# Performance work log

Hardware: AMD Instinct MI355X
Metric: run time of the kernel (lower is better)

## Reference

```python
import jax, jax.numpy as jnp
import numpy as np

PS = 3
B, C, H, W = 4, 256, 64, 64
IMG = 256
_MEAN = np.array([0.485, 0.456, 0.406], dtype=np.float32).reshape(1, 3, 1, 1)
_STD = np.array([0.229, 0.224, 0.225], dtype=np.float32).reshape(1, 3, 1, 1)


def setup_inputs() -> dict:
    key = jax.random.key(0)
    ks = jax.random.split(key, 16)
    d = {
        "dense_features1": jax.random.normal(ks[0], (B, C, H, W), jnp.float32),
        "dense_features2": jax.random.normal(ks[1], (B, C, H, W), jnp.float32),
        "img_ref_hr": jax.random.uniform(ks[2], (B, 3, IMG, IMG), jnp.float32),
        "w1_1": jax.random.normal(ks[3], (64, 3, 3, 3), jnp.float32) * 0.05,
        "b1_1": jnp.zeros((64,), jnp.float32),
        "w1_2": jax.random.normal(ks[4], (64, 64, 3, 3), jnp.float32) * 0.05,
        "b1_2": jnp.zeros((64,), jnp.float32),
        "w2_1": jax.random.normal(ks[5], (128, 64, 3, 3), jnp.float32) * 0.05,
        "b2_1": jnp.zeros((128,), jnp.float32),
        "w2_2": jax.random.normal(ks[6], (128, 128, 3, 3), jnp.float32) * 0.05,
        "b2_2": jnp.zeros((128,), jnp.float32),
        "w3_1": jax.random.normal(ks[7], (256, 128, 3, 3), jnp.float32) * 0.05,
        "b3_1": jnp.zeros((256,), jnp.float32),
    }
    return d


def _conv(x, w, b):
    y = jax.lax.conv_general_dilated(x, w, (1, 1), "SAME",
                                     dimension_numbers=("NCHW", "OIHW", "NCHW"))
    return y + b[None, :, None, None]


def _pool(x):
    return jax.lax.reduce_window(x, -jnp.inf, jax.lax.max, (1, 1, 2, 2), (1, 1, 2, 2), "VALID")


def _vgg(img, w11, b11, w12, b12, w21, b21, w22, b22, w31, b31):
    x = (img - _MEAN) / _STD  # ImageNet input norm (use_input_norm=True)
    r11 = jax.nn.relu(_conv(x, w11, b11))
    x = _pool(jax.nn.relu(_conv(r11, w12, b12)))
    r21 = jax.nn.relu(_conv(x, w21, b21))
    x = _pool(jax.nn.relu(_conv(r21, w22, b22)))
    r31 = jax.nn.relu(_conv(x, w31, b31))
    return r11, r21, r31


def _l2n(f):  # per-pixel channel L2 normalize (F.normalize dim=0, eps=1e-12)
    return f / jnp.maximum(jnp.linalg.norm(f, axis=0, keepdims=True), 1e-12)


def _patches(f):  # (c,h,w) -> (nh*nw, c*PS*PS), row-major patch order
    c, h, w = f.shape
    nh, nw = h - PS + 1, w - PS + 1
    cols = jnp.stack([f[:, i:i + nh, j:j + nw] for i in range(PS) for j in range(PS)], axis=1)
    return cols.reshape(c * PS * PS, nh * nw).T


def _match(fin, fref):
    fin, fref = _l2n(fin), _l2n(fref)
    nh, nw = fin.shape[1] - PS + 1, fin.shape[2] - PS + 1
    p_in = _patches(fin)
    p_ref = _patches(fref)
    p_ref = p_ref / (jnp.linalg.norm(p_ref, axis=1, keepdims=True) + 1e-5)  # is_norm
    corr = p_in @ p_ref.T  # (N_in, N_ref) patch correlation
    return jnp.argmax(corr, axis=1).reshape(nh, nw)


def _index_to_flow(idx):  # (nh,nw) int -> (nh+2, nw+2, 2) float flow
    nh, nw = idx.shape
    fw = (idx % nw).astype(jnp.float32) - jnp.arange(nw, dtype=jnp.float32)[None, :]
    fh = (idx // nw).astype(jnp.float32) - jnp.arange(nh, dtype=jnp.float32)[:, None]
    flow = jnp.stack([fw, fh], axis=-1)
    return jnp.pad(flow, ((0, 2), (0, 2), (0, 0)))


def _shift9(flow, s):  # 9 down/right shifts with zero fill -> (9,H,W,2)
    Hh, Ww, _ = flow.shape
    outs = [jnp.pad(flow, ((i * s, 0), (j * s, 0), (0, 0)))[:Hh, :Ww]
            for i in range(3) for j in range(3)]
    return jnp.stack(outs, axis=0)


def _per_sample(fin, fref):
    flow3 = _index_to_flow(_match(fin, fref))
    off3 = _shift9(flow3, 1)
    flow2 = jnp.repeat(jnp.repeat(flow3, 2, axis=0), 2, axis=1) * 2.0
    off2 = _shift9(flow2, 2)
    flow1 = jnp.repeat(jnp.repeat(flow3, 4, axis=0), 4, axis=1) * 4.0
    off1 = _shift9(flow1, 4)
    return off1, off2, off3


def reference(dense_features1, dense_features2, img_ref_hr,
              w1_1, b1_1, w1_2, b1_2, w2_1, b2_1, w2_2, b2_2, w3_1, b3_1):
    off1, off2, off3 = jax.vmap(_per_sample)(dense_features1, dense_features2)
    r11, r21, r31 = _vgg(img_ref_hr, w1_1, b1_1, w1_2, b1_2, w2_1, b2_1, w2_2, b2_2, w3_1, b3_1)
    # pre_offset['relu1_1'/'relu2_1'/'relu3_1'], img_ref_feat['relu1_1'/'relu2_1'/'relu3_1']
    return (off1, off2, off3, r11, r21, r31)
```

## Files before the change

### kernel.cpp

```cpp
#include <hip/hip_runtime.h>

typedef __attribute__((ext_vector_type(4))) float f32x4;
typedef __attribute__((ext_vector_type(8))) short s16x8;

#define OFF1_OFF 0
#define OFF2_OFF 4718592
#define OFF3_OFF 5898240
#define R11_OFF  6193152
#define R21_OFF  22970368
#define R31_OFF  31358976

__device__ __forceinline__ ushort f2bf(float x) {
  union { float f; uint u; } c; c.f = x;
  uint r = c.u + 0x7FFFu + ((c.u >> 16) & 1u);
  return (ushort)(r >> 16);
}
__device__ __forceinline__ float bfval(ushort h) {
  union { uint u; float f; } c; c.u = ((uint)h) << 16;
  return c.f;
}

__global__ __launch_bounds__(256)
void k_normalize(const float* __restrict__ f1, const float* __restrict__ f2,
                 ushort* __restrict__ n1b, ushort* __restrict__ n2b) {
  __shared__ uint ldsu[64 * 256];
  float* red = (float*)ldsu;
  float* inv = (float*)ldsu + 256;
  const int t = threadIdx.x, x = t & 63, cg = t >> 6;
  const int h = blockIdx.x, b = blockIdx.y;
  const float* in = blockIdx.z ? f2 : f1;
  ushort* op = blockIdx.z ? n2b : n1b;
  const size_t base = (size_t)b * 256 * 4096 + (size_t)h * 64 + x;
  float vals[64];
  float s = 0.f;
  #pragma unroll
  for (int ci = 0; ci < 64; ++ci) {
    float v = in[base + (size_t)(cg * 64 + ci) * 4096];
    vals[ci] = v;
    s = fmaf(v, v, s);
  }
  red[t] = s;
  __syncthreads();
  if (t < 64) {
    float tot = red[t] + red[64 + t] + red[128 + t] + red[192 + t];
    inv[t] = 1.0f / fmaxf(sqrtf(tot), 1e-12f);
  }
  __syncthreads();
  const float iv = inv[x];
  __syncthreads();
  #pragma unroll
  for (int j = 0; j < 32; ++j) {
    float v0 = vals[2 * j] * iv, v1 = vals[2 * j + 1] * iv;
    ushort h0 = f2bf(v0), h1 = f2bf(v1);
    ushort l0 = f2bf(v0 - bfval(h0)), l1 = f2bf(v1 - bfval(h1));
    int cc = (cg << 1) + (j >> 4);
    int i = j & 15;
    int qh = cc * 32 + i, ql = cc * 32 + 16 + i;
    ldsu[x * 256 + (qh ^ (x & 31))] = (uint)h0 | ((uint)h1 << 16);
    ldsu[x * 256 + (ql ^ (x & 31))] = (uint)l0 | ((uint)l1 << 16);
  }
  __syncthreads();
  uint* og = (uint*)(op + ((size_t)b * 4096 + h * 64) * 512);
  #pragma unroll
  for (int it = 0; it < 64; ++it) {
    int idx = it * 256 + t;
    int p = idx >> 8, q = idx & 255;
    og[idx] = ldsu[p * 256 + (q ^ (p & 31))];
  }
}

__global__ __launch_bounds__(256)
void k_pgemm_mfma(const ushort* __restrict__ Ab0, const ushort* __restrict__ Bb0,
                  float* __restrict__ P0) {
  __shared__ __align__(16) ushort As[128 * 64];
  __shared__ __align__(16) ushort Bs[128 * 64];
  const int t = threadIdx.x;
  const int bz = blockIdx.z;
  const ushort* Ab = Ab0 + (size_t)bz * 2097152;
  const ushort* Bb = Bb0 + (size_t)bz * 2097152;
  float* P = P0 + (size_t)bz * 16777216;
  const int u0 = blockIdx.y * 128, v0 = blockIdx.x * 128;
  const int lane = t & 63, wv = t >> 6;
  const int wm = wv >> 1, wn = wv & 1;
  const int lr = lane & 15, lk = lane >> 4;
  int rowv[4], slotv[4];
  #pragma unroll
  for (int i = 0; i < 4; ++i) { int e = t + i * 256; rowv[i] = e >> 3; slotv[i] = e & 7; }
  s16x8 ra[4], rb[4];
  #pragma unroll
  for (int i = 0; i < 4; ++i) {
    ra[i] = *(const s16x8*)(Ab + ((size_t)(u0 + rowv[i])) * 512 + slotv[i] * 8);
    rb[i] = *(const s16x8*)(Bb + ((size_t)(v0 + rowv[i])) * 512 + slotv[i] * 8);
  }
  f32x4 acc[4][4];
  #pragma unroll
  for (int mt = 0; mt < 4; ++mt)
    #pragma unroll
    for (int nt = 0; nt < 4; ++nt) {
      f32x4 z = {0.f, 0.f, 0.f, 0.f};
      acc[mt][nt] = z;
    }

  #pragma unroll 1
  for (int cc = 0; cc < 8; ++cc) {
    __syncthreads();
    #pragma unroll
    for (int i = 0; i < 4; ++i) {
      *(s16x8*)(As + ((rowv[i] << 3) + (slotv[i] ^ (rowv[i] & 7))) * 8) = ra[i];
      *(s16x8*)(Bs + ((rowv[i] << 3) + (slotv[i] ^ (rowv[i] & 7))) * 8) = rb[i];
    }
    __syncthreads();
    if (cc < 7) {
      #pragma unroll
      for (int i = 0; i < 4; ++i) {
        ra[i] = *(const s16x8*)(Ab + ((size_t)(u0 + rowv[i])) * 512 + (cc + 1) * 64 + slotv[i] * 8);
        rb[i] = *(const s16x8*)(Bb + ((size_t)(v0 + rowv[i])) * 512 + (cc + 1) * 64 + slotv[i] * 8);
      }
    }
    s16x8 ah[4], al[4], bh[4], bl[4];
    #pragma unroll
    for (int mt = 0; mt < 4; ++mt) {
      int row = wm * 64 + mt * 16 + lr;
      ah[mt] = *(const s16x8*)(As + ((row << 3) + (lk ^ (row & 7))) * 8);
      al[mt] = *(const s16x8*)(As + ((row << 3) + ((4 + lk) ^ (row & 7))) * 8);
    }
    #pragma unroll
    for (int nt = 0; nt < 4; ++nt) {
      int row = wn * 64 + nt * 16 + lr;
      bh[nt] = *(const s16x8*)(Bs + ((row << 3) + (lk ^ (row & 7))) * 8);
      bl[nt] = *(const s16x8*)(Bs + ((row << 3) + ((4 + lk) ^ (row & 7))) * 8);
    }
    #pragma unroll
    for (int mt = 0; mt < 4; ++mt)
      #pragma unroll
      for (int nt = 0; nt < 4; ++nt) {
        acc[mt][nt] = __builtin_amdgcn_mfma_f32_16x16x32_bf16(al[mt], bh[nt], acc[mt][nt], 0, 0, 0);
        acc[mt][nt] = __builtin_amdgcn_mfma_f32_16x16x32_bf16(ah[mt], bl[nt], acc[mt][nt], 0, 0, 0);
        acc[mt][nt] = __builtin_amdgcn_mfma_f32_16x16x32_bf16(ah[mt], bh[nt], acc[mt][nt], 0, 0, 0);
      }
  }
  const int plane = ((blockIdx.y * 2 + wm) << 6) + blockIdx.x * 2 + wn;
  float* Pp = P + (size_t)plane * 4096;
  #pragma unroll
  for (int mt = 0; mt < 4; ++mt)
    #pragma unroll
    for (int nt = 0; nt < 4; ++nt) {
      #pragma unroll
      for (int r = 0; r < 4; ++r)
        Pp[(mt * 16 + lk * 4 + r) * 64 + nt * 16 + lr] = acc[mt][nt][r];
    }
}

__global__ __launch_bounds__(256)
void k_corr(const float* __restrict__ P0, float* __restrict__ pv0,
            int* __restrict__ pi0) {
  __shared__ __align__(16) f32x4 Pl[3 * 1024];
  __shared__ float rv[256];
  __shared__ int   ri[256];
  const int t = threadIdx.x;
  const int orig = blockIdx.x;
  const int w = (orig & 7) * 1922 + (orig >> 3);
  const int bz = w / 3844;
  const int r2 = w % 3844;
  const int py = r2 / 62, qy = r2 % 62;
  const float* P = P0 + (size_t)bz * 16777216;
  float* pv = pv0 + (size_t)bz * 238328;
  int*   pi = pi0 + (size_t)bz * 238328;
  #pragma unroll
  for (int i = 0; i < 12; ++i) {
    int e = t + i * 256;
    int blk = e >> 10, rem = e & 1023;
    int px = rem >> 4, q4 = rem & 15;
    int pidx = (py + blk) * 64 + (qy + blk);
    f32x4 v = *(const f32x4*)(P + (size_t)pidx * 4096 + rem * 4);
    int slot = ((q4 + (px >> 4)) & 15) ^ (px & 15);
    Pl[blk * 1024 + px * 16 + slot] = v;
  }
  __syncthreads();
  const int px = t & 63, cg = t >> 6;
  #pragma unroll
  for (int j = 0; j < 4; ++j) {
    int c = cg * 4 + j;
    int slot = ((c + (px >> 4)) & 15) ^ (px & 15);
    int o = px * 16 + slot;
    Pl[o] = Pl[o] + Pl[1024 + o] + Pl[2048 + o];
  }
  __syncthreads();
  float bv = -3.4e38f; int bq = 0;
  if (px < 62) {
    const int q0 = cg * 16;
    const int nq = (cg < 3) ? 16 : 14;
    const int nch = (cg < 3) ? 5 : 4;
    float f[3][20];
    #pragma unroll
    for (int dj = 0; dj < 3; ++dj) {
      const int row = px + dj;
      const int rr = row >> 4, rm = row & 15;
      #pragma unroll
      for (int cc2 = 0; cc2 < 5; ++cc2) {
        if (cc2 < nch) {
          int c = cg * 4 + cc2;
          int slot = ((c + rr) & 15) ^ rm;
          f32x4 v = Pl[row * 16 + slot];
          f[dj][cc2 * 4 + 0] = v[0];
          f[dj][cc2 * 4 + 1] = v[1];
          f[dj][cc2 * 4 + 2] = v[2];
          f[dj][cc2 * 4 + 3] = v[3];
        }
      }
    }
    #pragma unroll
    for (int l = 0; l < 16; ++l) {
      if (l < nq) {
        float s = f[0][l] + f[1][l + 1] + f[2][l + 2];
        if (s > bv) { bv = s; bq = q0 + l; }
      }
    }
  }
  rv[t] = bv; ri[t] = bq;
  __syncthreads();
  if (t < 62) {
    float v = rv[t]; int q = ri[t];
    #pragma unroll
    for (int g = 1; g < 4; ++g) {
      float v2 = rv[g * 64 + t];
      if (v2 > v) { v = v2; q = ri[g * 64 + t]; }
    }
    const int n = py * 62 + t;
    pv[(size_t)n * 62 + qy] = v;
    pi[(size_t)n * 62 + qy] = qy * 62 + q;
  }
}

__global__ void k_argmax(const float* __restrict__ pv, const int* __restrict__ pi,
                         int* __restrict__ idxf) {
  int tid = blockIdx.x * 256 + threadIdx.x;
  if (tid >= 4 * 3844) return;
  const float* v = pv + (size_t)tid * 62;
  const int*  ii = pi + (size_t)tid * 62;
  float bv = v[0]; int bi = ii[0];
  for (int q = 1; q < 62; ++q) {
    float x = v[q];
    if (x > bv) { bv = x; bi = ii[q]; }
  }
  idxf[tid] = bi;
}

__global__ void k_flow_all(const int* __restrict__ idxf, float* __restrict__ out) {
  int gid = blockIdx.x * 256 + threadIdx.x;
  int Ho, lg, rel = gid;
  float* o;
  if (gid < 2359296)      { Ho = 256; lg = 2; o = out + OFF1_OFF; }
  else if (gid < 2949120) { Ho = 128; lg = 1; o = out + OFF2_OFF; rel -= 2359296; }
  else if (gid < 3096576) { Ho = 64;  lg = 0; o = out + OFF3_OFF; rel -= 2949120; }
  else return;
  const int x = rel % Ho;
  const int y = (rel / Ho) % Ho;
  const int s = (rel / (Ho * Ho)) % 9;
  const int b = rel / (Ho * Ho * 9);
  const int i = s / 3, j = s % 3;
  const int sc = 1 << lg;
  const int yy = y - i * sc, xx = x - j * sc;
  float fw = 0.f, fh = 0.f;
  if (yy >= 0 && xx >= 0) {
    const int r = yy >> lg, c = xx >> lg;
    if (r < 62 && c < 62) {
      const int id = idxf[b * 3844 + r * 62 + c];
      fw = (float)((id % 62 - c) * sc);
      fh = (float)((id / 62 - r) * sc);
    }
  }
  float2 ov = {fw, fh};
  *(float2*)(o + (size_t)rel * 2) = ov;
}

__global__ void k_wprep_all(const float* __restrict__ w12, const float* __restrict__ w21,
                            const float* __restrict__ w22, const float* __restrict__ w31,
                            ushort* __restrict__ o12, ushort* __restrict__ o21,
                            ushort* __restrict__ o22, ushort* __restrict__ o31) {
  int gid = blockIdx.x * 256 + threadIdx.x;
  const float* w; ushort* o; int CIN, rel;
  if (gid < 36864)        { w = w12; o = o12; CIN = 64;  rel = gid; }
  else if (gid < 110592)  { w = w21; o = o21; CIN = 64;  rel = gid - 36864; }
  else if (gid < 258048)  { w = w22; o = o22; CIN = 128; rel = gid - 110592; }
  else if (gid < 552960)  { w = w31; o = o31; CIN = 128; rel = gid - 258048; }
  else return;
  int ci = rel % CIN;
  int r = rel / CIN;
  int tap = r % 9;
  int oc = r / 9;
  o[((size_t)oc * 9 + tap) * CIN + ci] = f2bf(w[((size_t)oc * CIN + ci) * 9 + tap]);
}

__global__ void k_zb(ushort* __restrict__ a11, ushort* __restrict__ p1,
                     ushort* __restrict__ a21, ushort* __restrict__ p2) {
  int gid = blockIdx.x * 256 + threadIdx.x;
  if (gid >= 99072) return;
  int b = gid / 24768, r = gid % 24768;
  ushort* p; int Hp, Wp, C8, u;
  size_t stride;
  if (r < 8224)       { p = a11; Hp = 258; Wp = 258; C8 = 8;  stride = 4260096; u = r; }
  else if (r < 12352) { p = p1;  Hp = 130; Wp = 130; C8 = 8;  stride = 1081600; u = r - 8224; }
  else if (r < 20608) { p = a21; Hp = 130; Wp = 130; C8 = 16; stride = 2163200; u = r - 12352; }
  else                { p = p2;  Hp = 66;  Wp = 66;  C8 = 16; stride = 557568;  u = r - 20608; }
  int pos = u / C8, j = u % C8;
  int row, col;
  if (pos < Wp)            { row = 0;      col = pos; }
  else if (pos < 2 * Wp)   { row = Hp - 1; col = pos - Wp; }
  else { int q = pos - 2 * Wp; row = 1 + (q >> 1); col = (q & 1) ? (Wp - 1) : 0; }
  s16x8 z = {0, 0, 0, 0, 0, 0, 0, 0};
  *(s16x8*)(p + (size_t)b * stride + (((size_t)row * Wp + col) * C8 + j) * 8) = z;
}

__global__ __launch_bounds__(256)
void k_conv11(const float* __restrict__ img0, const float* __restrict__ w,
              const float* __restrict__ bias, float* __restrict__ outF0,
              ushort* __restrict__ outB0) {
  __shared__ float wl[1728];
  __shared__ float bl[64];
  const int t = threadIdx.x;
  const int b = blockIdx.y;
  const float* img = img0 + (size_t)b * 3 * 65536;
  float* outF = outF0 + (size_t)b * 64 * 65536;
  ushort* outB = outB0 + (size_t)b * 4260096;
  for (int i = t; i < 1728; i += 256) wl[i] = w[i];
  if (t < 64) bl[t] = bias[t];
  __syncthreads();
  const int x = t, y = blockIdx.x;
  const float mean[3] = {0.485f, 0.456f, 0.406f};
  const float stdv[3] = {0.229f, 0.224f, 0.225f};
  float v[27];
  #pragma unroll
  for (int c = 0; c < 3; ++c)
    #pragma unroll
    for (int dy = 0; dy < 3; ++dy)
      #pragma unroll
      for (int dx = 0; dx < 3; ++dx) {
        int iy = y + dy - 1, ix = x + dx - 1;
        float val = 0.f;
        if (iy >= 0 && iy < 256 && ix >= 0 && ix < 256)
          val = (img[((size_t)c * 256 + iy) * 256 + ix] - mean[c]) / stdv[c];
        v[c * 9 + dy * 3 + dx] = val;
      }
  float ov[64];
  #pragma unroll 4
  for (int oc = 0; oc < 64; ++oc) {
    float a = bl[oc];
    #pragma unroll
    for (int k = 0; k < 27; ++k) a = fmaf(wl[oc * 27 + k], v[k], a);
    a = fmaxf(a, 0.f);
    ov[oc] = a;
    outF[((size_t)oc * 256 + y) * 256 + x] = a;
  }
  uint* ob = (uint*)(outB + (((size_t)(y + 1) * 258 + (x + 1)) << 6));
  #pragma unroll
  for (int j = 0; j < 32; ++j)
    ob[j] = (uint)f2bf(ov[2 * j]) | ((uint)f2bf(ov[2 * j + 1]) << 16);
}

template <int CIN, bool POOL, bool WB16>
__global__ __launch_bounds__(256)
void k_mconv(const ushort* __restrict__ inb, const ushort* __restrict__ wB,
             const float* __restrict__ bias, float* __restrict__ outF,
             ushort* __restrict__ outB, int H, int W, int Cout,
             int inStride, int fStride, int bStride, int PW, int POut) {
  __shared__ __align__(16) char lds_raw[33792];
  ushort* As = (ushort*)lds_raw;
  float*  sm = (float*)lds_raw;
  const int t = threadIdx.x;
  const int bz = blockIdx.z;
  inb += (size_t)bz * inStride;
  outF += (size_t)bz * fStride;
  outB += (size_t)bz * bStride;
  const int xtiles = W >> 6;
  const int xt = blockIdx.x % xtiles;
  const int yp = blockIdx.x / xtiles;
  const int x0 = xt << 6, y0 = yp << 1;
  const int ocb = blockIdx.y << 6;
  const int lane = t & 63, wv = t >> 6;
  const int wm = wv >> 1, wn = wv & 1;
  const int lr = lane & 15, lk = lane >> 4;
  constexpr int NC2 = CIN / 64;

  f32x4 acc[4][2];
  #pragma unroll
  for (int mr = 0; mr < 4; ++mr)
    #pragma unroll
    for (int n = 0; n < 2; ++n) {
      f32x4 z = {0.f, 0.f, 0.f, 0.f};
      acc[mr][n] = z;
    }

  #pragma unroll 1
  for (int cc = 0; cc < NC2; ++cc) {
    __syncthreads();
    #pragma unroll
    for (int i = 0; i < 9; ++i) {
      int e = t + i * 256;
      if (e < 2112) {
        int pos = e >> 3;
        int gs = (e & 7) ^ (pos & 7);
        int hy = pos / 66, hx = pos - hy * 66;
        __builtin_amdgcn_global_load_lds(
            (const __attribute__((address_space(1))) void*)(
                inb + ((size_t)(y0 + hy) * PW + x0 + hx) * CIN + cc * 64 + gs * 8),
            (__attribute__((address_space(3))) void*)(As + (size_t)e * 8), 16, 0, 0);
      }
    }
    __syncthreads();
    #pragma unroll 3
    for (int tap = 0; tap < 9; ++tap) {
      const int dy = tap / 3, dx = tap % 3;
      s16x8 b0[2], b1[2];
      #pragma unroll
      for (int n = 0; n < 2; ++n) {
        const ushort* wp =
            wB + ((size_t)(ocb + wn * 32 + n * 16 + lr) * 9 + tap) * CIN + cc * 64 + lk * 8;
        b0[n] = *(const s16x8*)wp;
        b1[n] = *(const s16x8*)(wp + 32);
      }
      #pragma unroll
      for (int mr = 0; mr < 4; ++mr) {
        const int pos = (wm + dy) * 66 + mr * 16 + lr + dx;
        s16x8 a0 = *(const s16x8*)(As + ((pos << 3) + (lk ^ (pos & 7))) * 8);
        s16x8 a1 = *(const s16x8*)(As + ((pos << 3) + ((4 + lk) ^ (pos & 7))) * 8);
        #pragma unroll
        for (int n = 0; n < 2; ++n) {
          acc[mr][n] = __builtin_amdgcn_mfma_f32_16x16x32_bf16(a0, b0[n], acc[mr][n], 0, 0, 0);
          acc[mr][n] = __builtin_amdgcn_mfma_f32_16x16x32_bf16(a1, b1[n], acc[mr][n], 0, 0, 0);
        }
      }
    }
  }
  __syncthreads();
  #pragma unroll
  for (int mr = 0; mr < 4; ++mr)
    #pragma unroll
    for (int n = 0; n < 2; ++n) {
      const int oc = wn * 32 + n * 16 + lr;
      const float bs = bias[ocb + oc];
      #pragma unroll
      for (int r = 0; r < 4; ++r)
        sm[(wm * 64 + mr * 16 + lk * 4 + r) * 65 + oc] =
            fmaxf(acc[mr][n][r] + bs, 0.f);
    }
  __syncthreads();
  if (POOL) {
    #pragma unroll
    for (int i = 0; i < 4; ++i) {
      int e = t + i * 256;
      int op = e & 31, xo = e >> 5;
      int oc0 = op * 2;
      float m0 = fmaxf(fmaxf(sm[(xo * 2) * 65 + oc0], sm[(xo * 2 + 1) * 65 + oc0]),
                       fmaxf(sm[(64 + xo * 2) * 65 + oc0], sm[(64 + xo * 2 + 1) * 65 + oc0]));
      float m1 = fmaxf(fmaxf(sm[(xo * 2) * 65 + oc0 + 1], sm[(xo * 2 + 1) * 65 + oc0 + 1]),
                       fmaxf(sm[(64 + xo * 2) * 65 + oc0 + 1], sm[(64 + xo * 2 + 1) * 65 + oc0 + 1]));
      size_t pos = (size_t)(yp + 1) * POut + (x0 >> 1) + xo + 1;
      ((uint*)outB)[pos * (Cout >> 1) + ((ocb >> 1) + op)] =
          (uint)f2bf(m0) | ((uint)f2bf(m1) << 16);
    }
  } else {
    #pragma unroll
    for (int i = 0; i < 32; ++i) {
      int e = t + i * 256;
      int oc = e >> 7, sp = e & 127;
      outF[((size_t)(ocb + oc) * H + y0 + (sp >> 6)) * W + x0 + (sp & 63)] =
          sm[sp * 65 + oc];
    }
    if (WB16) {
      #pragma unroll
      for (int i = 0; i < 16; ++i) {
        int e = t + i * 256;
        int op = e & 31, sp = e >> 5;
        int oc0 = op * 2;
        float v0 = sm[sp * 65 + oc0], v1 = sm[sp * 65 + oc0 + 1];
        size_t pos = (size_t)(y0 + (sp >> 6) + 1) * POut + x0 + (sp & 63) + 1;
        ((uint*)outB)[pos * (Cout >> 1) + ((ocb >> 1) + op)] =
            (uint)f2bf(v0) | ((uint)f2bf(v1) << 16);
      }
    }
  }
}

extern "C" void kernel_launch(void* const* d_in, const int* in_sizes, int n_in,
                              void* d_out, int out_size, void* d_ws, size_t ws_size,
                              hipStream_t stream) {
  const float* df1 = (const float*)d_in[0];
  const float* df2 = (const float*)d_in[1];
  const float* img = (const float*)d_in[2];
  const float* w11 = (const float*)d_in[3];
  const float* b11 = (const float*)d_in[4];
  const float* w12 = (const float*)d_in[5];
  const float* b12 = (const float*)d_in[6];
  const float* w21 = (const float*)d_in[7];
  const float* b21 = (const float*)d_in[8];
  const float* w22 = (const float*)d_in[9];
  const float* b22 = (const float*)d_in[10];
  const float* w31 = (const float*)d_in[11];
  const float* b31 = (const float*)d_in[12];
  float* out = (float*)d_out;

  int* idxf = (int*)d_ws;
  ushort* w12b = (ushort*)(idxf + 15376);
  ushort* w21b = w12b + 36864;
  ushort* w22b = w21b + 73728;
  ushort* w31b = w22b + 147456;
  float* P4 = (float*)((char*)d_ws + (size_t)(4 << 20));
  ushort* a11s = (ushort*)P4;
  ushort* p1bs = a11s + 17040384;
  ushort* a21s = p1bs + 4326400;
  ushort* p2bs = a21s + 8652800;

  ushort* n1b = (ushort*)(out + R21_OFF);
  ushort* n2b = n1b + 8388608;
  float* pv = out + OFF1_OFF;
  int*   pi = (int*)(out + OFF1_OFF + 953312);

  k_normalize<<<dim3(64, 4, 2), 256, 0, stream>>>(df1, df2, n1b, n2b);
  k_wprep_all<<<2160, 256, 0, stream>>>(w12, w21, w22, w31, w12b, w21b, w22b, w31b);

  k_pgemm_mfma<<<dim3(32, 32, 4), 256, 0, stream>>>(n1b, n2b, P4);
  k_corr<<<15376, 256, 0, stream>>>(P4, pv, pi);
  k_argmax<<<61, 256, 0, stream>>>(pv, pi, idxf);

  k_zb<<<387, 256, 0, stream>>>(a11s, p1bs, a21s, p2bs);
  k_conv11<<<dim3(256, 4), 256, 0, stream>>>(img, w11, b11, out + R11_OFF, a11s);
  k_mconv<64, true, false><<<dim3(512, 1, 4), 256, 0, stream>>>(
      a11s, w12b, b12, nullptr, p1bs, 256, 256, 64, 4260096, 0, 1081600, 258, 130);
  k_mconv<64, false, true><<<dim3(128, 2, 4), 256, 0, stream>>>(
      p1bs, w21b, b21, out + R21_OFF, a21s, 128, 128, 128, 1081600, 2097152, 2163200, 130, 130);
  k_mconv<128, true, false><<<dim3(128, 2, 4), 256, 0, stream>>>(
      a21s, w22b, b22, nullptr, p2bs, 128, 128, 128, 2163200, 0, 557568, 130, 66);
  k_mconv<128, false, false><<<dim3(32, 4, 4), 256, 0, stream>>>(
      p2bs, w31b, b31, out + R31_OFF, nullptr, 64, 64, 256, 557568, 1048576, 0, 66, 0);

  k_flow_all<<<12096, 256, 0, stream>>>(idxf, out);
}
```

Baseline: 451.6 us.

## Double-buffer pgemm via direct global-to-LDS loads; coalesce conv11 bf16 stores through LDS

The correlation GEMM now stages A/B tiles with global_load_lds into two LDS buffers, prefetching two k-chunks ahead and waiting on vmcnt, instead of a register round-trip. This is meant to overlap global loads with MFMA work and remove the register-to-LDS copy. In conv11, the bf16 padded output is first gathered in a swizzled LDS buffer and then written out as coalesced 16-byte stores, replacing per-thread scattered 32-word writes. The cost is more LDS use, which can lower occupancy, and the vmcnt counting depends on the exact number of loads in flight.

```diff
diff --git a/kernel.cpp b/kernel.cpp
--- a/kernel.cpp
+++ b/kernel.cpp
@@ -72,26 +72,33 @@
 __global__ __launch_bounds__(256)
 void k_pgemm_mfma(const ushort* __restrict__ Ab0, const ushort* __restrict__ Bb0,
                   float* __restrict__ P0) {
-  __shared__ __align__(16) ushort As[128 * 64];
-  __shared__ __align__(16) ushort Bs[128 * 64];
+  __shared__ __align__(16) ushort As[2][8192];
+  __shared__ __align__(16) ushort Bs[2][8192];
   const int t = threadIdx.x;
   const int bz = blockIdx.z;
-  const ushort* Ab = Ab0 + (size_t)bz * 2097152;
-  const ushort* Bb = Bb0 + (size_t)bz * 2097152;
+  const ushort* Ab = Ab0 + (size_t)bz * 2097152 + (size_t)blockIdx.y * 128 * 512;
+  const ushort* Bb = Bb0 + (size_t)bz * 2097152 + (size_t)blockIdx.x * 128 * 512;
   float* P = P0 + (size_t)bz * 16777216;
-  const int u0 = blockIdx.y * 128, v0 = blockIdx.x * 128;
   const int lane = t & 63, wv = t >> 6;
   const int wm = wv >> 1, wn = wv & 1;
   const int lr = lane & 15, lk = lane >> 4;
-  int rowv[4], slotv[4];
-  #pragma unroll
-  for (int i = 0; i < 4; ++i) { int e = t + i * 256; rowv[i] = e >> 3; slotv[i] = e & 7; }
-  s16x8 ra[4], rb[4];
-  #pragma unroll
-  for (int i = 0; i < 4; ++i) {
-    ra[i] = *(const s16x8*)(Ab + ((size_t)(u0 + rowv[i])) * 512 + slotv[i] * 8);
-    rb[i] = *(const s16x8*)(Bb + ((size_t)(v0 + rowv[i])) * 512 + slotv[i] * 8);
-  }
+
+#define STAGE(buf, cc)                                                          \
+  do {                                                                          \
+    _Pragma("unroll")                                                           \
+    for (int j = 0; j < 4; ++j) {                                               \
+      int u = t + j * 256;                                                      \
+      int row = u >> 3;                                                         \
+      int gs = (u & 7) ^ (row & 7);                                             \
+      __builtin_amdgcn_global_load_lds(                                         \
+          (const __attribute__((address_space(1))) void*)(Ab + (size_t)row * 512 + (cc) * 64 + gs * 8), \
+          (__attribute__((address_space(3))) void*)(&As[buf][u * 8]), 16, 0, 0); \
+      __builtin_amdgcn_global_load_lds(                                         \
+          (const __attribute__((address_space(1))) void*)(Bb + (size_t)row * 512 + (cc) * 64 + gs * 8), \
+          (__attribute__((address_space(3))) void*)(&Bs[buf][u * 8]), 16, 0, 0); \
+    }                                                                           \
+  } while (0)
+
   f32x4 acc[4][4];
   #pragma unroll
   for (int mt = 0; mt < 4; ++mt)
@@ -101,34 +108,30 @@
       acc[mt][nt] = z;
     }
 
-  #pragma unroll 1
+  STAGE(0, 0);
+  STAGE(1, 1);
+
+  #pragma unroll
   for (int cc = 0; cc < 8; ++cc) {
-    __syncthreads();
-    #pragma unroll
-    for (int i = 0; i < 4; ++i) {
-      *(s16x8*)(As + ((rowv[i] << 3) + (slotv[i] ^ (rowv[i] & 7))) * 8) = ra[i];
-      *(s16x8*)(Bs + ((rowv[i] << 3) + (slotv[i] ^ (rowv[i] & 7))) * 8) = rb[i];
-    }
-    __syncthreads();
-    if (cc < 7) {
-      #pragma unroll
-      for (int i = 0; i < 4; ++i) {
-        ra[i] = *(const s16x8*)(Ab + ((size_t)(u0 + rowv[i])) * 512 + (cc + 1) * 64 + slotv[i] * 8);
-        rb[i] = *(const s16x8*)(Bb + ((size_t)(v0 + rowv[i])) * 512 + (cc + 1) * 64 + slotv[i] * 8);
-      }
-    }
+    const int cur = cc & 1;
+    if (cc < 7) { asm volatile("s_waitcnt vmcnt(8)" ::: "memory"); }
+    else        { asm volatile("s_waitcnt vmcnt(0)" ::: "memory"); }
+    __builtin_amdgcn_s_barrier();
+    __builtin_amdgcn_sched_barrier(0);
+    const ushort* Asb = As[cur];
+    const ushort* Bsb = Bs[cur];
     s16x8 ah[4], al[4], bh[4], bl[4];
     #pragma unroll
     for (int mt = 0; mt < 4; ++mt) {
       int row = wm * 64 + mt * 16 + lr;
-      ah[mt] = *(const s16x8*)(As + ((row << 3) + (lk ^ (row & 7))) * 8);
-      al[mt] = *(const s16x8*)(As + ((row << 3) + ((4 + lk) ^ (row & 7))) * 8);
+      ah[mt] = *(const s16x8*)(Asb + ((row << 3) + (lk ^ (row & 7))) * 8);
+      al[mt] = *(const s16x8*)(Asb + ((row << 3) + ((4 + lk) ^ (row & 7))) * 8);
     }
     #pragma unroll
     for (int nt = 0; nt < 4; ++nt) {
       int row = wn * 64 + nt * 16 + lr;
-      bh[nt] = *(const s16x8*)(Bs + ((row << 3) + (lk ^ (row & 7))) * 8);
-      bl[nt] = *(const s16x8*)(Bs + ((row << 3) + ((4 + lk) ^ (row & 7))) * 8);
+      bh[nt] = *(const s16x8*)(Bsb + ((row << 3) + (lk ^ (row & 7))) * 8);
+      bl[nt] = *(const s16x8*)(Bsb + ((row << 3) + ((4 + lk) ^ (row & 7))) * 8);
     }
     #pragma unroll
     for (int mt = 0; mt < 4; ++mt)
@@ -138,7 +141,12 @@
         acc[mt][nt] = __builtin_amdgcn_mfma_f32_16x16x32_bf16(ah[mt], bl[nt], acc[mt][nt], 0, 0, 0);
         acc[mt][nt] = __builtin_amdgcn_mfma_f32_16x16x32_bf16(ah[mt], bh[nt], acc[mt][nt], 0, 0, 0);
       }
-  }
+    __builtin_amdgcn_sched_barrier(0);
+    __builtin_amdgcn_s_barrier();
+    if (cc < 6) STAGE(cur, cc + 2);
+  }
+#undef STAGE
+
   const int plane = ((blockIdx.y * 2 + wm) << 6) + blockIdx.x * 2 + wn;
   float* Pp = P + (size_t)plane * 4096;
   #pragma unroll
@@ -318,6 +326,7 @@
               ushort* __restrict__ outB0) {
   __shared__ float wl[1728];
   __shared__ float bl[64];
+  __shared__ uint ob[8192];
   const int t = threadIdx.x;
   const int b = blockIdx.y;
   const float* img = img0 + (size_t)b * 3 * 65536;
@@ -342,20 +351,34 @@
           val = (img[((size_t)c * 256 + iy) * 256 + ix] - mean[c]) / stdv[c];
         v[c * 9 + dy * 3 + dx] = val;
       }
-  float ov[64];
+  const int xs = x & 31;
   #pragma unroll 4
-  for (int oc = 0; oc < 64; ++oc) {
-    float a = bl[oc];
-    #pragma unroll
-    for (int k = 0; k < 27; ++k) a = fmaf(wl[oc * 27 + k], v[k], a);
-    a = fmaxf(a, 0.f);
-    ov[oc] = a;
-    outF[((size_t)oc * 256 + y) * 256 + x] = a;
-  }
-  uint* ob = (uint*)(outB + (((size_t)(y + 1) * 258 + (x + 1)) << 6));
-  #pragma unroll
-  for (int j = 0; j < 32; ++j)
-    ob[j] = (uint)f2bf(ov[2 * j]) | ((uint)f2bf(ov[2 * j + 1]) << 16);
+  for (int op = 0; op < 32; ++op) {
+    float a0 = bl[2 * op], a1 = bl[2 * op + 1];
+    #pragma unroll
+    for (int k = 0; k < 27; ++k) a0 = fmaf(wl[(2 * op) * 27 + k], v[k], a0);
+    #pragma unroll
+    for (int k = 0; k < 27; ++k) a1 = fmaf(wl[(2 * op + 1) * 27 + k], v[k], a1);
+    a0 = fmaxf(a0, 0.f); a1 = fmaxf(a1, 0.f);
+    outF[((size_t)(2 * op) * 256 + y) * 256 + x] = a0;
+    outF[((size_t)(2 * op + 1) * 256 + y) * 256 + x] = a1;
+    ob[x * 32 + (op ^ xs)] = (uint)f2bf(a0) | ((uint)f2bf(a1) << 16);
+  }
+  __syncthreads();
+  uint* og = (uint*)(outB + (((size_t)(y + 1) * 258 + 1) << 6));
+  #pragma unroll
+  for (int it = 0; it < 8; ++it) {
+    int g4 = t + it * 256;
+    int xx = g4 >> 3;
+    int j0 = (g4 & 7) * 4;
+    int xs2 = xx & 31;
+    uint4 val;
+    val.x = ob[xx * 32 + ((j0 + 0) ^ xs2)];
+    val.y = ob[xx * 32 + ((j0 + 1) ^ xs2)];
+    val.z = ob[xx * 32 + ((j0 + 2) ^ xs2)];
+    val.w = ob[xx * 32 + ((j0 + 3) ^ xs2)];
+    *(uint4*)(og + (size_t)g4 * 4) = val;
+  }
 }
 
 template <int CIN, bool POOL, bool WB16>
```

Measured after the change: 408.0 us. -9.7%, faster.

## Walk correlation diagonals with a rolling 3-plane LDS buffer; stage conv11 bf16 stores

Applied to the files above, without the earlier changes.

k_corr now assigns each block a segment of up to 16 consecutive (py, qy) pairs along one diagonal. It keeps a rolling ring of three P planes in LDS, so each step loads one new plane, prefetched into registers, instead of three. This is meant to cut global reads of the 64MB P buffer roughly threefold, at the cost of fewer blocks (123x4x4 grid) and serialized steps per block. Separately, k_conv11 stages its bf16 output through a swizzled LDS tile and writes it back with coalesced 16-byte stores instead of strided per-thread 4-byte stores.

```diff
diff --git a/kernel.cpp b/kernel.cpp
--- a/kernel.cpp
+++ b/kernel.cpp
@@ -151,6 +151,7 @@
     }
 }
 
+#define SEG 16
 __global__ __launch_bounds__(256)
 void k_corr(const float* __restrict__ P0, float* __restrict__ pv0,
             int* __restrict__ pi0) {
@@ -158,77 +159,104 @@
   __shared__ float rv[256];
   __shared__ int   ri[256];
   const int t = threadIdx.x;
-  const int orig = blockIdx.x;
-  const int w = (orig & 7) * 1922 + (orig >> 3);
-  const int bz = w / 3844;
-  const int r2 = w % 3844;
-  const int py = r2 / 62, qy = r2 % 62;
+  const int d = (int)blockIdx.x - 61;
+  const int seg = blockIdx.y, bz = blockIdx.z;
+  const int lo = d > 0 ? d : 0;
+  const int hi = d > 0 ? 61 : 61 + d;
+  const int py0 = lo + seg * SEG;
+  if (py0 > hi) return;
+  const int pyE = min(py0 + SEG - 1, hi);
   const float* P = P0 + (size_t)bz * 16777216;
   float* pv = pv0 + (size_t)bz * 238328;
   int*   pi = pi0 + (size_t)bz * 238328;
-  #pragma unroll
-  for (int i = 0; i < 12; ++i) {
+
+  int stg_off[4];
+  #pragma unroll
+  for (int i = 0; i < 4; ++i) {
     int e = t + i * 256;
-    int blk = e >> 10, rem = e & 1023;
-    int px = rem >> 4, q4 = rem & 15;
-    int pidx = (py + blk) * 64 + (qy + blk);
-    f32x4 v = *(const f32x4*)(P + (size_t)pidx * 4096 + rem * 4);
-    int slot = ((q4 + (px >> 4)) & 15) ^ (px & 15);
-    Pl[blk * 1024 + px * 16 + slot] = v;
-  }
-  __syncthreads();
+    int spx = e >> 4, sq4 = e & 15;
+    stg_off[i] = spx * 16 + (((sq4 + (spx >> 4)) & 15) ^ (spx & 15));
+  }
+  #pragma unroll 1
+  for (int k = 0; k < 3; ++k) {
+    const int a = py0 + k;
+    const float* Pp = P + (size_t)(a * 64 + (a - d)) * 4096;
+    #pragma unroll
+    for (int i = 0; i < 4; ++i)
+      Pl[k * 1024 + stg_off[i]] = *(const f32x4*)(Pp + (t + i * 256) * 4);
+  }
   const int px = t & 63, cg = t >> 6;
-  #pragma unroll
-  for (int j = 0; j < 4; ++j) {
-    int c = cg * 4 + j;
-    int slot = ((c + (px >> 4)) & 15) ^ (px & 15);
-    int o = px * 16 + slot;
-    Pl[o] = Pl[o] + Pl[1024 + o] + Pl[2048 + o];
-  }
-  __syncthreads();
-  float bv = -3.4e38f; int bq = 0;
-  if (px < 62) {
-    const int q0 = cg * 16;
-    const int nq = (cg < 3) ? 16 : 14;
-    const int nch = (cg < 3) ? 5 : 4;
-    float f[3][20];
-    #pragma unroll
-    for (int dj = 0; dj < 3; ++dj) {
-      const int row = px + dj;
-      const int rr = row >> 4, rm = row & 15;
-      #pragma unroll
-      for (int cc2 = 0; cc2 < 5; ++cc2) {
-        if (cc2 < nch) {
-          int c = cg * 4 + cc2;
-          int slot = ((c + rr) & 15) ^ rm;
-          f32x4 v = Pl[row * 16 + slot];
-          f[dj][cc2 * 4 + 0] = v[0];
-          f[dj][cc2 * 4 + 1] = v[1];
-          f[dj][cc2 * 4 + 2] = v[2];
-          f[dj][cc2 * 4 + 3] = v[3];
+  int cur = 0;
+  #pragma unroll 1
+  for (int py = py0; py <= pyE; ++py) {
+    const int qy = py - d;
+    const bool havenext = (py < pyE);
+    f32x4 pf[4];
+    if (havenext) {
+      const int a = py + 3;
+      const float* Pp = P + (size_t)(a * 64 + (a - d)) * 4096;
+      #pragma unroll
+      for (int i = 0; i < 4; ++i) pf[i] = *(const f32x4*)(Pp + (t + i * 256) * 4);
+    }
+    __syncthreads();
+    f32x4* b0 = Pl + cur * 1024;
+    const f32x4* b1 = Pl + ((cur + 1) % 3) * 1024;
+    const f32x4* b2 = Pl + ((cur + 2) % 3) * 1024;
+    #pragma unroll
+    for (int i = 0; i < 4; ++i) {
+      int o = stg_off[i];
+      b0[o] = b0[o] + b1[o] + b2[o];
+    }
+    __syncthreads();
+    float bv = -3.4e38f; int bq = 0;
+    if (px < 62) {
+      const int q0 = cg * 16;
+      const int nq = (cg < 3) ? 16 : 14;
+      const int nch = (cg < 3) ? 5 : 4;
+      float f[3][20];
+      #pragma unroll
+      for (int dj = 0; dj < 3; ++dj) {
+        const int row = px + dj;
+        const int rr = row >> 4, rm = row & 15;
+        #pragma unroll
+        for (int cc2 = 0; cc2 < 5; ++cc2) {
+          if (cc2 < nch) {
+            int c = cg * 4 + cc2;
+            int slot = ((c + rr) & 15) ^ rm;
+            f32x4 v = b0[row * 16 + slot];
+            f[dj][cc2 * 4 + 0] = v[0];
+            f[dj][cc2 * 4 + 1] = v[1];
+            f[dj][cc2 * 4 + 2] = v[2];
+            f[dj][cc2 * 4 + 3] = v[3];
+          }
         }
       }
-    }
-    #pragma unroll
-    for (int l = 0; l < 16; ++l) {
-      if (l < nq) {
-        float s = f[0][l] + f[1][l + 1] + f[2][l + 2];
-        if (s > bv) { bv = s; bq = q0 + l; }
-      }
-    }
-  }
-  rv[t] = bv; ri[t] = bq;
-  __syncthreads();
-  if (t < 62) {
-    float v = rv[t]; int q = ri[t];
-    #pragma unroll
-    for (int g = 1; g < 4; ++g) {
-      float v2 = rv[g * 64 + t];
-      if (v2 > v) { v = v2; q = ri[g * 64 + t]; }
-    }
-    const int n = py * 62 + t;
-    pv[(size_t)n * 62 + qy] = v;
-    pi[(size_t)n * 62 + qy] = qy * 62 + q;
+      #pragma unroll
+      for (int l = 0; l < 16; ++l) {
+        if (l < nq) {
+          float s = f[0][l] + f[1][l + 1] + f[2][l + 2];
+          if (s > bv) { bv = s; bq = q0 + l; }
+        }
+      }
+    }
+    rv[t] = bv; ri[t] = bq;
+    __syncthreads();
+    if (t < 62) {
+      float v = rv[t]; int q = ri[t];
+      #pragma unroll
+      for (int g = 1; g < 4; ++g) {
+        float v2 = rv[g * 64 + t];
+        if (v2 > v) { v = v2; q = ri[g * 64 + t]; }
+      }
+      const int n = py * 62 + t;
+      pv[(size_t)n * 62 + qy] = v;
+      pi[(size_t)n * 62 + qy] = qy * 62 + q;
+    }
+    if (havenext) {
+      #pragma unroll
+      for (int i = 0; i < 4; ++i) b0[stg_off[i]] = pf[i];
+    }
+    cur = (cur + 1) % 3;
   }
 }
 
@@ -318,6 +346,7 @@
               ushort* __restrict__ outB0) {
   __shared__ float wl[1728];
   __shared__ float bl[64];
+  __shared__ uint ob[8192];
   const int t = threadIdx.x;
   const int b = blockIdx.y;
   const float* img = img0 + (size_t)b * 3 * 65536;
@@ -342,20 +371,34 @@
           val = (img[((size_t)c * 256 + iy) * 256 + ix] - mean[c]) / stdv[c];
         v[c * 9 + dy * 3 + dx] = val;
       }
-  float ov[64];
+  const int xs = x & 31;
   #pragma unroll 4
-  for (int oc = 0; oc < 64; ++oc) {
-    float a = bl[oc];
-    #pragma unroll
-    for (int k = 0; k < 27; ++k) a = fmaf(wl[oc * 27 + k], v[k], a);
-    a = fmaxf(a, 0.f);
-    ov[oc] = a;
-    outF[((size_t)oc * 256 + y) * 256 + x] = a;
-  }
-  uint* ob = (uint*)(outB + (((size_t)(y + 1) * 258 + (x + 1)) << 6));
-  #pragma unroll
-  for (int j = 0; j < 32; ++j)
-    ob[j] = (uint)f2bf(ov[2 * j]) | ((uint)f2bf(ov[2 * j + 1]) << 16);
+  for (int op = 0; op < 32; ++op) {
+    float a0 = bl[2 * op], a1 = bl[2 * op + 1];
+    #pragma unroll
+    for (int k = 0; k < 27; ++k) a0 = fmaf(wl[(2 * op) * 27 + k], v[k], a0);
+    #pragma unroll
+    for (int k = 0; k < 27; ++k) a1 = fmaf(wl[(2 * op + 1) * 27 + k], v[k], a1);
+    a0 = fmaxf(a0, 0.f); a1 = fmaxf(a1, 0.f);
+    outF[((size_t)(2 * op) * 256 + y) * 256 + x] = a0;
+    outF[((size_t)(2 * op + 1) * 256 + y) * 256 + x] = a1;
+    ob[x * 32 + (op ^ xs)] = (uint)f2bf(a0) | ((uint)f2bf(a1) << 16);
+  }
+  __syncthreads();
+  uint* og = (uint*)(outB + (((size_t)(y + 1) * 258 + 1) << 6));
+  #pragma unroll
+  for (int it = 0; it < 8; ++it) {
+    int g4 = t + it * 256;
+    int xx = g4 >> 3;
+    int j0 = (g4 & 7) * 4;
+    int xs2 = xx & 31;
+    uint4 val;
+    val.x = ob[xx * 32 + ((j0 + 0) ^ xs2)];
+    val.y = ob[xx * 32 + ((j0 + 1) ^ xs2)];
+    val.z = ob[xx * 32 + ((j0 + 2) ^ xs2)];
+    val.w = ob[xx * 32 + ((j0 + 3) ^ xs2)];
+    *(uint4*)(og + (size_t)g4 * 4) = val;
+  }
 }
 
 template <int CIN, bool POOL, bool WB16>
@@ -520,7 +563,7 @@
   k_wprep_all<<<2160, 256, 0, stream>>>(w12, w21, w22, w31, w12b, w21b, w22b, w31b);
 
   k_pgemm_mfma<<<dim3(32, 32, 4), 256, 0, stream>>>(n1b, n2b, P4);
-  k_corr<<<15376, 256, 0, stream>>>(P4, pv, pi);
+  k_corr<<<dim3(123, 4, 4), 256, 0, stream>>>(P4, pv, pi);
   k_argmax<<<61, 256, 0, stream>>>(pv, pi, idxf);
 
   k_zb<<<387, 256, 0, stream>>>(a11s, p1bs, a21s, p2bs);
```

Result: faster. 420.5 us (-6.9%).

## Process correlation per batch to keep P in cache; stage conv11 bf16 output in LDS

Applied to the files above, without the earlier changes.

The batched correlation GEMM and corr launches become a loop of four per-sample launches that reuse one 64 MB P buffer. The intent is for P to stay resident in the large last-level cache between the GEMM write and the corr read, instead of a 256 MB buffer going round trip through HBM. This adds launches and serialises the samples, which lowers parallelism per launch. Separately, conv11 now stages its bf16 output through swizzled LDS so the global writes are coalesced 16-byte stores rather than per-thread strided 32 uint stores.

```diff
diff --git a/kernel.cpp b/kernel.cpp
--- a/kernel.cpp
+++ b/kernel.cpp
@@ -70,15 +70,11 @@
 }
 
 __global__ __launch_bounds__(256)
-void k_pgemm_mfma(const ushort* __restrict__ Ab0, const ushort* __restrict__ Bb0,
-                  float* __restrict__ P0) {
+void k_pgemm_mfma(const ushort* __restrict__ Ab, const ushort* __restrict__ Bb,
+                  float* __restrict__ P) {
   __shared__ __align__(16) ushort As[128 * 64];
   __shared__ __align__(16) ushort Bs[128 * 64];
   const int t = threadIdx.x;
-  const int bz = blockIdx.z;
-  const ushort* Ab = Ab0 + (size_t)bz * 2097152;
-  const ushort* Bb = Bb0 + (size_t)bz * 2097152;
-  float* P = P0 + (size_t)bz * 16777216;
   const int u0 = blockIdx.y * 128, v0 = blockIdx.x * 128;
   const int lane = t & 63, wv = t >> 6;
   const int wm = wv >> 1, wn = wv & 1;
@@ -152,20 +148,13 @@
 }
 
 __global__ __launch_bounds__(256)
-void k_corr(const float* __restrict__ P0, float* __restrict__ pv0,
-            int* __restrict__ pi0) {
+void k_corr(const float* __restrict__ P, float* __restrict__ pv,
+            int* __restrict__ pi) {
   __shared__ __align__(16) f32x4 Pl[3 * 1024];
   __shared__ float rv[256];
   __shared__ int   ri[256];
   const int t = threadIdx.x;
-  const int orig = blockIdx.x;
-  const int w = (orig & 7) * 1922 + (orig >> 3);
-  const int bz = w / 3844;
-  const int r2 = w % 3844;
-  const int py = r2 / 62, qy = r2 % 62;
-  const float* P = P0 + (size_t)bz * 16777216;
-  float* pv = pv0 + (size_t)bz * 238328;
-  int*   pi = pi0 + (size_t)bz * 238328;
+  const int py = blockIdx.x / 62, qy = blockIdx.x % 62;
   #pragma unroll
   for (int i = 0; i < 12; ++i) {
     int e = t + i * 256;
@@ -318,6 +307,7 @@
               ushort* __restrict__ outB0) {
   __shared__ float wl[1728];
   __shared__ float bl[64];
+  __shared__ uint ob[8192];
   const int t = threadIdx.x;
   const int b = blockIdx.y;
   const float* img = img0 + (size_t)b * 3 * 65536;
@@ -342,20 +332,34 @@
           val = (img[((size_t)c * 256 + iy) * 256 + ix] - mean[c]) / stdv[c];
         v[c * 9 + dy * 3 + dx] = val;
       }
-  float ov[64];
+  const int xs = x & 31;
   #pragma unroll 4
-  for (int oc = 0; oc < 64; ++oc) {
-    float a = bl[oc];
-    #pragma unroll
-    for (int k = 0; k < 27; ++k) a = fmaf(wl[oc * 27 + k], v[k], a);
-    a = fmaxf(a, 0.f);
-    ov[oc] = a;
-    outF[((size_t)oc * 256 + y) * 256 + x] = a;
-  }
-  uint* ob = (uint*)(outB + (((size_t)(y + 1) * 258 + (x + 1)) << 6));
-  #pragma unroll
-  for (int j = 0; j < 32; ++j)
-    ob[j] = (uint)f2bf(ov[2 * j]) | ((uint)f2bf(ov[2 * j + 1]) << 16);
+  for (int op = 0; op < 32; ++op) {
+    float a0 = bl[2 * op], a1 = bl[2 * op + 1];
+    #pragma unroll
+    for (int k = 0; k < 27; ++k) a0 = fmaf(wl[(2 * op) * 27 + k], v[k], a0);
+    #pragma unroll
+    for (int k = 0; k < 27; ++k) a1 = fmaf(wl[(2 * op + 1) * 27 + k], v[k], a1);
+    a0 = fmaxf(a0, 0.f); a1 = fmaxf(a1, 0.f);
+    outF[((size_t)(2 * op) * 256 + y) * 256 + x] = a0;
+    outF[((size_t)(2 * op + 1) * 256 + y) * 256 + x] = a1;
+    ob[x * 32 + (op ^ xs)] = (uint)f2bf(a0) | ((uint)f2bf(a1) << 16);
+  }
+  __syncthreads();
+  uint* og = (uint*)(outB + (((size_t)(y + 1) * 258 + 1) << 6));
+  #pragma unroll
+  for (int it = 0; it < 8; ++it) {
+    int g4 = t + it * 256;
+    int xx = g4 >> 3;
+    int j0 = (g4 & 7) * 4;
+    int xs2 = xx & 31;
+    uint4 val;
+    val.x = ob[xx * 32 + ((j0 + 0) ^ xs2)];
+    val.y = ob[xx * 32 + ((j0 + 1) ^ xs2)];
+    val.z = ob[xx * 32 + ((j0 + 2) ^ xs2)];
+    val.w = ob[xx * 32 + ((j0 + 3) ^ xs2)];
+    *(uint4*)(og + (size_t)g4 * 4) = val;
+  }
 }
 
 template <int CIN, bool POOL, bool WB16>
@@ -505,8 +509,8 @@
   ushort* w21b = w12b + 36864;
   ushort* w22b = w21b + 73728;
   ushort* w31b = w22b + 147456;
-  float* P4 = (float*)((char*)d_ws + (size_t)(4 << 20));
-  ushort* a11s = (ushort*)P4;
+  float* P = (float*)((char*)d_ws + (size_t)(4 << 20));
+  ushort* a11s = (ushort*)P;
   ushort* p1bs = a11s + 17040384;
   ushort* a21s = p1bs + 4326400;
   ushort* p2bs = a21s + 8652800;
@@ -519,8 +523,12 @@
   k_normalize<<<dim3(64, 4, 2), 256, 0, stream>>>(df1, df2, n1b, n2b);
   k_wprep_all<<<2160, 256, 0, stream>>>(w12, w21, w22, w31, w12b, w21b, w22b, w31b);
 
-  k_pgemm_mfma<<<dim3(32, 32, 4), 256, 0, stream>>>(n1b, n2b, P4);
-  k_corr<<<15376, 256, 0, stream>>>(P4, pv, pi);
+  for (int b = 0; b < 4; ++b) {
+    k_pgemm_mfma<<<dim3(32, 32, 1), 256, 0, stream>>>(
+        n1b + (size_t)b * 2097152, n2b + (size_t)b * 2097152, P);
+    k_corr<<<3844, 256, 0, stream>>>(P, pv + (size_t)b * 238328,
+                                     pi + (size_t)b * 238328);
+  }
   k_argmax<<<61, 256, 0, stream>>>(pv, pi, idxf);
 
   k_zb<<<387, 256, 0, stream>>>(a11s, p1bs, a21s, p2bs);
```

Result: slower. 469.9 us (+4.0%).
